# Kernel tuning notes

Measured on AMD Instinct MI355X. Metric: run time of the kernel, lower is better.

The kernel has to match this reference:

```python
import jax, jax.numpy as jnp
import numpy as np

NEG_SLOPE = 0.2  # PyG GATv2Conv default negative_slope


def gatv2_layer(x, Wl, Wr, att, bias, src, dst, N, H, C):
    # x: [N, F_in]; Wl, Wr: [F_in, H*C]; att: [H, C]; bias: [H*C]
    xl = (x @ Wl).reshape(N, H, C)  # source transform (lin_l)
    xr = (x @ Wr).reshape(N, H, C)  # target transform (lin_r)
    # per-edge GATv2 score: a^T LeakyReLU(xl[j] + xr[i])
    e = jax.nn.leaky_relu(xl[src] + xr[dst], NEG_SLOPE)      # [E, H, C]
    logits = jnp.einsum('ehc,hc->eh', e, att)                # [E, H]
    # segment softmax over incoming edges of each destination node
    m = jax.ops.segment_max(logits, dst, num_segments=N)     # [N, H]
    p = jnp.exp(logits - m[dst])                             # [E, H]
    s = jax.ops.segment_sum(p, dst, num_segments=N)          # [N, H]
    alpha = p / s[dst]                                       # [E, H]
    out = jax.ops.segment_sum(xl[src] * alpha[..., None], dst, num_segments=N)  # [N, H, C]
    return out.reshape(N, H * C) + bias


def setup_inputs() -> dict:
    key = jax.random.key(0)
    ks = jax.random.split(key, 12)
    B, N, F_IN = 1, 100000, 128
    E, H, C = 1600000, 4, 16
    D = H * C  # 64
    x = jax.random.normal(ks[0], (B, N, F_IN), dtype=jnp.float32)
    edge_index = jax.random.randint(ks[1], (2, E), 0, N, dtype=jnp.int32)
    def glorot(k, shape):
        fan_in, fan_out = shape[0], shape[1]
        lim = (6.0 / (fan_in + fan_out)) ** 0.5
        return jax.random.uniform(k, shape, jnp.float32, -lim, lim)
    # layer 1: F_IN -> H*C ; layer 2: H*C -> H*C
    W1l = glorot(ks[2], (F_IN, D))
    W1r = glorot(ks[3], (F_IN, D))
    att1 = glorot(ks[4], (H, C))
    b1 = jnp.zeros((D,), jnp.float32)
    W2l = glorot(ks[5], (D, D))
    W2r = glorot(ks[6], (D, D))
    att2 = glorot(ks[7], (H, C))
    b2 = jnp.zeros((D,), jnp.float32)
    return {"x": x, "edge_index": edge_index,
            "W1l": W1l, "W1r": W1r, "att1": att1, "b1": b1,
            "W2l": W2l, "W2r": W2r, "att2": att2, "b2": b2}


def reference(x, edge_index, W1l, W1r, att1, b1, W2l, W2r, att2, b2):
    B, N_per, F = x.shape
    N = B * N_per
    H, C = att1.shape
    h = x.reshape(N, F)
    # PyG GATv2Conv adds self-loops by default
    loops = jnp.arange(N, dtype=edge_index.dtype)
    src = jnp.concatenate([edge_index[0], loops])
    dst = jnp.concatenate([edge_index[1], loops])
    h = jax.nn.relu(gatv2_layer(h, W1l, W1r, att1, b1, src, dst, N, H, C))
    # dropout is identity in eval mode
    h = jax.nn.relu(gatv2_layer(h, W2l, W2r, att2, b2, src, dst, N, H, C))
    return h.reshape(B, N_per, -1)
```

## Files before the change

### kernel.cpp

```cpp
#include <hip/hip_runtime.h>
#include <hip/hip_bf16.h>


typedef unsigned long long u64;

#define NBLK_S 512
#define LOG2E 1.44269504f

template <int CTRL>
__device__ __forceinline__ float add_ror(float v) {
    int r = __builtin_amdgcn_update_dpp(0, __float_as_int(v), CTRL, 0xF, 0xF, true);
    return v + __int_as_float(r);
}
__device__ __forceinline__ float head_sum16(float v) {
    v = add_ror<0x121>(v);
    v = add_ror<0x122>(v);
    v = add_ror<0x124>(v);
    v = add_ror<0x128>(v);
    return v;
}

__global__ void hist_kernel(const int* __restrict__ dst, int* __restrict__ deg, int E) {
    int i = blockIdx.x * blockDim.x + threadIdx.x;
    int stride = gridDim.x * blockDim.x;
    for (; i < E; i += stride) atomicAdd(&deg[dst[i]], 1);
}

__global__ void scan_a(const int* __restrict__ deg, int* __restrict__ incl,
                       int* __restrict__ partials, int n) {
    __shared__ int sm[2][1024];
    int tid = threadIdx.x;
    int i = blockIdx.x * 1024 + tid;
    int v = (i < n) ? deg[i] : 0;
    sm[0][tid] = v;
    __syncthreads();
    int pin = 0;
    #pragma unroll
    for (int ofs = 1; ofs < 1024; ofs <<= 1) {
        int pout = pin ^ 1;
        sm[pout][tid] = sm[pin][tid] + ((tid >= ofs) ? sm[pin][tid - ofs] : 0);
        pin = pout;
        __syncthreads();
    }
    int r = sm[pin][tid];
    if (i < n) incl[i] = r;
    if (tid == 1023) partials[blockIdx.x] = r;
}

__global__ void scan_b(int* partials, int nblk) {
    __shared__ int sm[2][1024];
    int tid = threadIdx.x;
    int v = (tid < nblk) ? partials[tid] : 0;
    sm[0][tid] = v;
    __syncthreads();
    int pin = 0;
    #pragma unroll
    for (int ofs = 1; ofs < 1024; ofs <<= 1) {
        int pout = pin ^ 1;
        sm[pout][tid] = sm[pin][tid] + ((tid >= ofs) ? sm[pin][tid - ofs] : 0);
        pin = pout;
        __syncthreads();
    }
    if (tid < nblk) partials[tid] = sm[pin][tid] - v;
}

__global__ void scan_c(const int* __restrict__ deg, const int* __restrict__ incl,
                       const int* __restrict__ partials, int* __restrict__ offs,
                       int n, int E) {
    int i = blockIdx.x * blockDim.x + threadIdx.x;
    if (i < n) offs[i] = partials[i >> 10] + incl[i] - deg[i];
    if (i == 0) offs[n] = E;
}

__global__ __launch_bounds__(256) void sort_hist(const int* __restrict__ edst,
                                                 int* __restrict__ gh, int E, int nW) {
    __shared__ int h[256];
    for (int i = threadIdx.x; i < nW; i += 256) h[i] = 0;
    __syncthreads();
    const int chunk = (E + NBLK_S - 1) / NBLK_S;
    const int lo = blockIdx.x * chunk;
    const int hi = min(E, lo + chunk);
    for (int i = lo + threadIdx.x; i < hi; i += 256)
        atomicAdd(&h[edst[i] >> 9], 1);
    __syncthreads();
    for (int w = threadIdx.x; w < nW; w += 256)
        gh[w * NBLK_S + blockIdx.x] = h[w];
}

__global__ __launch_bounds__(NBLK_S) void sort_scan(const int* __restrict__ offs,
                                                    int* __restrict__ gh, int N) {
    __shared__ int sm[2][NBLK_S];
    const int w = blockIdx.x;
    const int t = threadIdx.x;
    int v = gh[w * NBLK_S + t];
    sm[0][t] = v;
    __syncthreads();
    int pin = 0;
    #pragma unroll
    for (int ofs = 1; ofs < NBLK_S; ofs <<= 1) {
        int pout = pin ^ 1;
        sm[pout][t] = sm[pin][t] + ((t >= ofs) ? sm[pin][t - ofs] : 0);
        pin = pout;
        __syncthreads();
    }
    gh[w * NBLK_S + t] = offs[w << 9] + sm[pin][t] - v;
}

__global__ __launch_bounds__(256) void sort_place(const int* __restrict__ esrc,
                                                  const int* __restrict__ edst,
                                                  const int* __restrict__ gh,
                                                  u64* __restrict__ pairs, int E, int nW) {
    __shared__ int cur[256];
    for (int i = threadIdx.x; i < nW; i += 256)
        cur[i] = gh[i * NBLK_S + blockIdx.x];
    __syncthreads();
    const int chunk = (E + NBLK_S - 1) / NBLK_S;
    const int lo = blockIdx.x * chunk;
    const int hi = min(E, lo + chunk);
    for (int i = lo + threadIdx.x; i < hi; i += 256) {
        int d = edst[i];
        int s = esrc[i];
        int pos = atomicAdd(&cur[d >> 9], 1);
        pairs[pos] = ((u64)(unsigned)d << 32) | (unsigned)s;
    }
}

__global__ __launch_bounds__(256) void window_scatter(const u64* __restrict__ pairs,
                                                      const int* __restrict__ offs,
                                                      int* __restrict__ srcs, int N) {
    __shared__ int cur[512];
    int w = blockIdx.x;
    int d0 = w << 9;
    int nd = min(512, N - d0);
    for (int i = threadIdx.x; i < nd; i += 256) cur[i] = offs[d0 + i];
    __syncthreads();
    int p0 = offs[d0];
    int p1 = offs[min(d0 + 512, N)];
    for (int idx = p0 + threadIdx.x; idx < p1; idx += 256) {
        u64 pr = pairs[idx];
        int d = (int)(pr >> 32);
        int s = (int)(pr & 0xffffffffu);
        int pos = atomicAdd(&cur[d - d0], 1);
        srcs[pos] = s;
    }
}

#define WIDX(c) ((c) + (((c) >> 5) << 2))
template <int K>
__global__ __launch_bounds__(256) void gemm_lr(const float* __restrict__ X,
                                               const float* __restrict__ Wl,
                                               const float* __restrict__ Wr,
                                               float* __restrict__ xl,
                                               float* __restrict__ xr, int N) {
    constexpr int KT = 64;
    constexpr int LDW = 140;
    constexpr int LDX = KT + 4;
    __shared__ float Ws[KT][LDW];
    __shared__ float Xs[64][LDX];
    const int tid = threadIdx.x;
    const int rbase = blockIdx.x * 64;
    const int tx = tid & 15;
    const int ty = tid >> 4;
    const int c0 = tx * 8;
    const int wc = WIDX(c0);

    float acc[4][8];
    #pragma unroll
    for (int j = 0; j < 4; ++j)
        #pragma unroll
        for (int i = 0; i < 8; ++i) acc[j][i] = 0.f;

    #pragma unroll
    for (int t = 0; t < K / KT; ++t) {
        if (t) __syncthreads();
        for (int f = tid; f < KT * 16; f += 256) {
            int k = f >> 4;
            int c = (f & 15) << 2;
            float4 a = *reinterpret_cast<const float4*>(&Wl[(size_t)(t * KT + k) * 64 + c]);
            float4 b = *reinterpret_cast<const float4*>(&Wr[(size_t)(t * KT + k) * 64 + c]);
            *reinterpret_cast<float4*>(&Ws[k][WIDX(c)]) = a;
            *reinterpret_cast<float4*>(&Ws[k][WIDX(64 + c)]) = b;
        }
        for (int f = tid; f < 64 * (KT / 4); f += 256) {
            int m = f >> 4;
            int k4 = (f & 15) << 2;
            int r = rbase + m;
            float4 v = (r < N) ? *reinterpret_cast<const float4*>(&X[(size_t)r * K + t * KT + k4])
                               : make_float4(0.f, 0.f, 0.f, 0.f);
            *reinterpret_cast<float4*>(&Xs[m][k4]) = v;
        }
        __syncthreads();

        #pragma unroll 2
        for (int k4 = 0; k4 < KT; k4 += 4) {
            float4 xv[4];
            #pragma unroll
            for (int j = 0; j < 4; ++j)
                xv[j] = *reinterpret_cast<const float4*>(&Xs[ty + 16 * j][k4]);
            #pragma unroll
            for (int kk = 0; kk < 4; ++kk) {
                float4 w0 = *reinterpret_cast<const float4*>(&Ws[k4 + kk][wc]);
                float4 w1 = *reinterpret_cast<const float4*>(&Ws[k4 + kk][wc + 4]);
                float w[8] = {w0.x, w0.y, w0.z, w0.w, w1.x, w1.y, w1.z, w1.w};
                #pragma unroll
                for (int j = 0; j < 4; ++j) {
                    float xk = (kk == 0) ? xv[j].x : (kk == 1) ? xv[j].y
                             : (kk == 2) ? xv[j].z : xv[j].w;
                    #pragma unroll
                    for (int i = 0; i < 8; ++i)
                        acc[j][i] = fmaf(xk, w[i], acc[j][i]);
                }
            }
        }
    }

    float* op = (c0 < 64) ? xl : xr;
    const int cc = c0 & 63;
    #pragma unroll
    for (int j = 0; j < 4; ++j) {
        int r = rbase + ty + 16 * j;
        if (r < N) {
            float4 v0 = make_float4(acc[j][0], acc[j][1], acc[j][2], acc[j][3]);
            float4 v1 = make_float4(acc[j][4], acc[j][5], acc[j][6], acc[j][7]);
            *reinterpret_cast<float4*>(&op[(size_t)r * 64 + cc]) = v0;
            *reinterpret_cast<float4*>(&op[(size_t)r * 64 + cc + 4]) = v1;
        }
    }
}

__global__ __launch_bounds__(256) void gat_kernel(const float* __restrict__ xl,
                                                  const float* __restrict__ xr,
                                                  const int* __restrict__ offs,
                                                  const int* __restrict__ srcs,
                                                  const float* __restrict__ att,
                                                  const float* __restrict__ bias,
                                                  float* __restrict__ out, int N) {
    int lane = threadIdx.x & 63;
    int wid = threadIdx.x >> 6;
    int n = blockIdx.x * 4 + wid;
    if (n >= N) return;
    float att_l = att[lane] * LOG2E;
    float b_l = bias[lane];
    float xr_d = xr[(size_t)n * 64 + lane];
    float xls = xl[(size_t)n * 64 + lane];
    float v = xls + xr_d;
    float p = exp2f(head_sum16(att_l * fmaxf(v, 0.2f * v)));
    float s0 = p, s1 = 0.f, s2 = 0.f, s3 = 0.f;
    float o0 = xls * p, o1 = 0.f, o2 = 0.f, o3 = 0.f;
    int e0 = offs[n], e1 = offs[n + 1];
    int j = e0;
    for (; j + 3 < e1; j += 4) {
        int sa = srcs[j], sb = srcs[j + 1], sc = srcs[j + 2], sd = srcs[j + 3];
        float xa = xl[(size_t)sa * 64 + lane];
        float xb = xl[(size_t)sb * 64 + lane];
        float xc = xl[(size_t)sc * 64 + lane];
        float xd = xl[(size_t)sd * 64 + lane];
        float ua = xa + xr_d, ub = xb + xr_d, uc = xc + xr_d, ud = xd + xr_d;
        float pa = exp2f(head_sum16(att_l * fmaxf(ua, 0.2f * ua)));
        float pb = exp2f(head_sum16(att_l * fmaxf(ub, 0.2f * ub)));
        float pc = exp2f(head_sum16(att_l * fmaxf(uc, 0.2f * uc)));
        float pd = exp2f(head_sum16(att_l * fmaxf(ud, 0.2f * ud)));
        s0 += pa; s1 += pb; s2 += pc; s3 += pd;
        o0 = fmaf(xa, pa, o0);
        o1 = fmaf(xb, pb, o1);
        o2 = fmaf(xc, pc, o2);
        o3 = fmaf(xd, pd, o3);
    }
    for (; j < e1; ++j) {
        int sa = srcs[j];
        float xa = xl[(size_t)sa * 64 + lane];
        float ua = xa + xr_d;
        float pa = exp2f(head_sum16(att_l * fmaxf(ua, 0.2f * ua)));
        s1 += pa;
        o1 = fmaf(xa, pa, o1);
    }
    float s = (s0 + s1) + (s2 + s3);
    float o = (o0 + o1) + (o2 + o3);
    out[(size_t)n * 64 + lane] = fmaxf(o / s + b_l, 0.f);
}

extern "C" void kernel_launch(void* const* d_in, const int* in_sizes, int n_in,
                              void* d_out, int out_size, void* d_ws, size_t ws_size,
                              hipStream_t stream) {
    const float* x    = (const float*)d_in[0];
    const int*   edge = (const int*)d_in[1];
    const float* W1l  = (const float*)d_in[2];
    const float* W1r  = (const float*)d_in[3];
    const float* att1 = (const float*)d_in[4];
    const float* b1   = (const float*)d_in[5];
    const float* W2l  = (const float*)d_in[6];
    const float* W2r  = (const float*)d_in[7];
    const float* att2 = (const float*)d_in[8];
    const float* b2   = (const float*)d_in[9];

    const int N = in_sizes[0] / 128;
    const int E = in_sizes[1] / 2;
    const int* esrc = edge;
    const int* edst = edge + E;

    char* ws = (char*)d_ws;
    size_t off = 0;
    auto alloc = [&](size_t bytes) {
        void* p = ws + off;
        off += (bytes + 255) & ~(size_t)255;
        return p;
    };
    float* xl     = (float*)alloc((size_t)N * 64 * 4);
    float* xr     = (float*)alloc((size_t)N * 64 * 4);
    float* h      = (float*)alloc((size_t)N * 64 * 4);
    int* deg      = (int*)alloc((size_t)N * 4);
    int* incl     = (int*)alloc((size_t)N * 4);
    int* offs     = (int*)alloc((size_t)(N + 1) * 4);
    int* partials = (int*)alloc(1024 * 4);
    int* srcs     = (int*)alloc((size_t)E * 4);
    u64* pairs    = (u64*)alloc((size_t)E * 8);
    int* gh       = (int*)alloc((size_t)256 * NBLK_S * 4);
    (void)ws_size;

    hipMemsetAsync(deg, 0, (size_t)N * 4, stream);

    const int nblk = (N + 1023) >> 10;
    const int nW = (N + 511) >> 9;
    hist_kernel<<<1024, 256, 0, stream>>>(edst, deg, E);
    scan_a<<<nblk, 1024, 0, stream>>>(deg, incl, partials, N);
    scan_b<<<1, 1024, 0, stream>>>(partials, nblk);
    scan_c<<<(N + 255) / 256, 256, 0, stream>>>(deg, incl, partials, offs, N, E);
    sort_hist<<<NBLK_S, 256, 0, stream>>>(edst, gh, E, nW);
    sort_scan<<<nW, NBLK_S, 0, stream>>>(offs, gh, N);
    sort_place<<<NBLK_S, 256, 0, stream>>>(esrc, edst, gh, pairs, E, nW);
    window_scatter<<<nW, 256, 0, stream>>>(pairs, offs, srcs, N);

    const int gblk = (N + 63) / 64;
    gemm_lr<128><<<gblk, 256, 0, stream>>>(x, W1l, W1r, xl, xr, N);
    gat_kernel<<<(N + 3) / 4, 256, 0, stream>>>(xl, xr, offs, srcs, att1, b1, h, N);
    gemm_lr<64><<<gblk, 256, 0, stream>>>(h, W2l, W2r, xl, xr, N);
    gat_kernel<<<(N + 3) / 4, 256, 0, stream>>>(xl, xr, offs, srcs, att2, b2, (float*)d_out, N);
}
```

Baseline: 461.5 us.

## Fuse histograms, overlap edge sort with first GEMM, compact pairs, tune GAT gather

```diff
diff --git a/kernel.cpp b/kernel.cpp
--- a/kernel.cpp
+++ b/kernel.cpp
@@ -20,10 +20,23 @@
     return v;
 }
 
-__global__ void hist_kernel(const int* __restrict__ dst, int* __restrict__ deg, int E) {
-    int i = blockIdx.x * blockDim.x + threadIdx.x;
-    int stride = gridDim.x * blockDim.x;
-    for (; i < E; i += stride) atomicAdd(&deg[dst[i]], 1);
+__global__ __launch_bounds__(256) void hist_fused(const int* __restrict__ edst,
+                                                  int* __restrict__ deg,
+                                                  int* __restrict__ gh, int E, int nW) {
+    __shared__ int h[256];
+    for (int i = threadIdx.x; i < 256; i += 256) h[i] = 0;
+    __syncthreads();
+    const int chunk = (E + NBLK_S - 1) / NBLK_S;
+    const int lo = blockIdx.x * chunk;
+    const int hi = min(E, lo + chunk);
+    for (int i = lo + threadIdx.x; i < hi; i += 256) {
+        int d = edst[i];
+        atomicAdd(&deg[d], 1);
+        atomicAdd(&h[d >> 9], 1);
+    }
+    __syncthreads();
+    for (int w = threadIdx.x; w < nW; w += 256)
+        gh[w * NBLK_S + blockIdx.x] = h[w];
 }
 
 __global__ void scan_a(const int* __restrict__ deg, int* __restrict__ incl,
@@ -72,21 +85,6 @@
     if (i == 0) offs[n] = E;
 }
 
-__global__ __launch_bounds__(256) void sort_hist(const int* __restrict__ edst,
-                                                 int* __restrict__ gh, int E, int nW) {
-    __shared__ int h[256];
-    for (int i = threadIdx.x; i < nW; i += 256) h[i] = 0;
-    __syncthreads();
-    const int chunk = (E + NBLK_S - 1) / NBLK_S;
-    const int lo = blockIdx.x * chunk;
-    const int hi = min(E, lo + chunk);
-    for (int i = lo + threadIdx.x; i < hi; i += 256)
-        atomicAdd(&h[edst[i] >> 9], 1);
-    __syncthreads();
-    for (int w = threadIdx.x; w < nW; w += 256)
-        gh[w * NBLK_S + blockIdx.x] = h[w];
-}
-
 __global__ __launch_bounds__(NBLK_S) void sort_scan(const int* __restrict__ offs,
                                                     int* __restrict__ gh, int N) {
     __shared__ int sm[2][NBLK_S];
@@ -106,59 +104,22 @@
     gh[w * NBLK_S + t] = offs[w << 9] + sm[pin][t] - v;
 }
 
-__global__ __launch_bounds__(256) void sort_place(const int* __restrict__ esrc,
-                                                  const int* __restrict__ edst,
-                                                  const int* __restrict__ gh,
-                                                  u64* __restrict__ pairs, int E, int nW) {
-    __shared__ int cur[256];
-    for (int i = threadIdx.x; i < nW; i += 256)
-        cur[i] = gh[i * NBLK_S + blockIdx.x];
-    __syncthreads();
-    const int chunk = (E + NBLK_S - 1) / NBLK_S;
-    const int lo = blockIdx.x * chunk;
-    const int hi = min(E, lo + chunk);
-    for (int i = lo + threadIdx.x; i < hi; i += 256) {
-        int d = edst[i];
-        int s = esrc[i];
-        int pos = atomicAdd(&cur[d >> 9], 1);
-        pairs[pos] = ((u64)(unsigned)d << 32) | (unsigned)s;
-    }
-}
-
-__global__ __launch_bounds__(256) void window_scatter(const u64* __restrict__ pairs,
-                                                      const int* __restrict__ offs,
-                                                      int* __restrict__ srcs, int N) {
-    __shared__ int cur[512];
-    int w = blockIdx.x;
-    int d0 = w << 9;
-    int nd = min(512, N - d0);
-    for (int i = threadIdx.x; i < nd; i += 256) cur[i] = offs[d0 + i];
-    __syncthreads();
-    int p0 = offs[d0];
-    int p1 = offs[min(d0 + 512, N)];
-    for (int idx = p0 + threadIdx.x; idx < p1; idx += 256) {
-        u64 pr = pairs[idx];
-        int d = (int)(pr >> 32);
-        int s = (int)(pr & 0xffffffffu);
-        int pos = atomicAdd(&cur[d - d0], 1);
-        srcs[pos] = s;
-    }
-}
-
 #define WIDX(c) ((c) + (((c) >> 5) << 2))
+#define GEMM_LDS_FLOATS (64 * 140 + 64 * 68)
+
 template <int K>
-__global__ __launch_bounds__(256) void gemm_lr(const float* __restrict__ X,
-                                               const float* __restrict__ Wl,
-                                               const float* __restrict__ Wr,
-                                               float* __restrict__ xl,
-                                               float* __restrict__ xr, int N) {
+__device__ __forceinline__ void gemm_body(int rbase, const float* __restrict__ X,
+                                          const float* __restrict__ Wl,
+                                          const float* __restrict__ Wr,
+                                          float* __restrict__ xl,
+                                          float* __restrict__ xr, int N,
+                                          float* __restrict__ sm) {
     constexpr int KT = 64;
     constexpr int LDW = 140;
     constexpr int LDX = KT + 4;
-    __shared__ float Ws[KT][LDW];
-    __shared__ float Xs[64][LDX];
+    float* Ws = sm;
+    float* Xs = sm + KT * LDW;
     const int tid = threadIdx.x;
-    const int rbase = blockIdx.x * 64;
     const int tx = tid & 15;
     const int ty = tid >> 4;
     const int c0 = tx * 8;
@@ -178,8 +139,8 @@
             int c = (f & 15) << 2;
             float4 a = *reinterpret_cast<const float4*>(&Wl[(size_t)(t * KT + k) * 64 + c]);
             float4 b = *reinterpret_cast<const float4*>(&Wr[(size_t)(t * KT + k) * 64 + c]);
-            *reinterpret_cast<float4*>(&Ws[k][WIDX(c)]) = a;
-            *reinterpret_cast<float4*>(&Ws[k][WIDX(64 + c)]) = b;
+            *reinterpret_cast<float4*>(&Ws[k * LDW + WIDX(c)]) = a;
+            *reinterpret_cast<float4*>(&Ws[k * LDW + WIDX(64 + c)]) = b;
         }
         for (int f = tid; f < 64 * (KT / 4); f += 256) {
             int m = f >> 4;
@@ -187,7 +148,7 @@
             int r = rbase + m;
             float4 v = (r < N) ? *reinterpret_cast<const float4*>(&X[(size_t)r * K + t * KT + k4])
                                : make_float4(0.f, 0.f, 0.f, 0.f);
-            *reinterpret_cast<float4*>(&Xs[m][k4]) = v;
+            *reinterpret_cast<float4*>(&Xs[m * LDX + k4]) = v;
         }
         __syncthreads();
 
@@ -196,11 +157,11 @@
             float4 xv[4];
             #pragma unroll
             for (int j = 0; j < 4; ++j)
-                xv[j] = *reinterpret_cast<const float4*>(&Xs[ty + 16 * j][k4]);
+                xv[j] = *reinterpret_cast<const float4*>(&Xs[(ty + 16 * j) * LDX + k4]);
             #pragma unroll
             for (int kk = 0; kk < 4; ++kk) {
-                float4 w0 = *reinterpret_cast<const float4*>(&Ws[k4 + kk][wc]);
-                float4 w1 = *reinterpret_cast<const float4*>(&Ws[k4 + kk][wc + 4]);
+                float4 w0 = *reinterpret_cast<const float4*>(&Ws[(k4 + kk) * LDW + wc]);
+                float4 w1 = *reinterpret_cast<const float4*>(&Ws[(k4 + kk) * LDW + wc + 4]);
                 float w[8] = {w0.x, w0.y, w0.z, w0.w, w1.x, w1.y, w1.z, w1.w};
                 #pragma unroll
                 for (int j = 0; j < 4; ++j) {
@@ -226,6 +187,77 @@
             *reinterpret_cast<float4*>(&op[(size_t)r * 64 + cc + 4]) = v1;
         }
     }
+}
+
+__global__ __launch_bounds__(256) void place_gemm(const int* __restrict__ esrc,
+                                                  const int* __restrict__ edst,
+                                                  const int* __restrict__ gh,
+                                                  unsigned* __restrict__ pairs,
+                                                  int E, int nW,
+                                                  const float* __restrict__ X,
+                                                  const float* __restrict__ Wl,
+                                                  const float* __restrict__ Wr,
+                                                  float* __restrict__ xl,
+                                                  float* __restrict__ xr, int N) {
+    __shared__ float sm[GEMM_LDS_FLOATS];
+    if (blockIdx.x < NBLK_S) {
+        int* cur = (int*)sm;
+        const int bid = blockIdx.x;
+        for (int i = threadIdx.x; i < nW; i += 256)
+            cur[i] = gh[i * NBLK_S + bid];
+        __syncthreads();
+        const int chunk = (E + NBLK_S - 1) / NBLK_S;
+        const int lo = bid * chunk;
+        const int hi = min(E, lo + chunk);
+        for (int i = lo + threadIdx.x; i < hi; i += 256) {
+            int d = edst[i];
+            int s = esrc[i];
+            int pos = atomicAdd(&cur[d >> 9], 1);
+            pairs[pos] = ((unsigned)(d & 511) << 17) | (unsigned)s;
+        }
+    } else {
+        gemm_body<128>((blockIdx.x - NBLK_S) * 64, X, Wl, Wr, xl, xr, N, sm);
+    }
+}
+
+__global__ __launch_bounds__(256) void scatter_gemm(const unsigned* __restrict__ pairs,
+                                                    const int* __restrict__ offs,
+                                                    int* __restrict__ srcs, int nW, int gemmBase,
+                                                    const float* __restrict__ X,
+                                                    const float* __restrict__ Wl,
+                                                    const float* __restrict__ Wr,
+                                                    float* __restrict__ xl,
+                                                    float* __restrict__ xr, int N) {
+    __shared__ float sm[GEMM_LDS_FLOATS];
+    if ((int)blockIdx.x < nW) {
+        int* cur = (int*)sm;
+        int w = blockIdx.x;
+        int d0 = w << 9;
+        int nd = min(512, N - d0);
+        for (int i = threadIdx.x; i < nd; i += 256) cur[i] = offs[d0 + i];
+        __syncthreads();
+        int p0 = offs[d0];
+        int p1 = offs[min(d0 + 512, N)];
+        for (int idx = p0 + threadIdx.x; idx < p1; idx += 256) {
+            unsigned pr = pairs[idx];
+            int doff = (int)(pr >> 17);
+            int s = (int)(pr & 0x1FFFFu);
+            int pos = atomicAdd(&cur[doff], 1);
+            srcs[pos] = s << 6;
+        }
+    } else {
+        gemm_body<128>((gemmBase + blockIdx.x - nW) * 64, X, Wl, Wr, xl, xr, N, sm);
+    }
+}
+
+template <int K>
+__global__ __launch_bounds__(256) void gemm_lr(const float* __restrict__ X,
+                                               const float* __restrict__ Wl,
+                                               const float* __restrict__ Wr,
+                                               float* __restrict__ xl,
+                                               float* __restrict__ xr, int N) {
+    __shared__ float sm[GEMM_LDS_FLOATS];
+    gemm_body<K>(blockIdx.x * 64, X, Wl, Wr, xl, xr, N, sm);
 }
 
 __global__ __launch_bounds__(256) void gat_kernel(const float* __restrict__ xl,
@@ -239,27 +271,39 @@
     int wid = threadIdx.x >> 6;
     int n = blockIdx.x * 4 + wid;
     if (n >= N) return;
-    float att_l = att[lane] * LOG2E;
+    float a_l = att[lane] * LOG2E;
+    float a1 = 0.6f * a_l;
+    float a2 = 0.4f * a_l;
     float b_l = bias[lane];
-    float xr_d = xr[(size_t)n * 64 + lane];
-    float xls = xl[(size_t)n * 64 + lane];
-    float v = xls + xr_d;
-    float p = exp2f(head_sum16(att_l * fmaxf(v, 0.2f * v)));
+    unsigned bn = (unsigned)n * 64u + (unsigned)lane;
+    float xr_d = xr[bn];
+    float xls = xl[bn];
+    float u = xls + xr_d;
+    float p = exp2f(head_sum16(fmaf(a1, u, a2 * fabsf(u))));
     float s0 = p, s1 = 0.f, s2 = 0.f, s3 = 0.f;
     float o0 = xls * p, o1 = 0.f, o2 = 0.f, o3 = 0.f;
     int e0 = offs[n], e1 = offs[n + 1];
     int j = e0;
+    int ja = min((e0 + 3) & ~3, e1);
+    for (; j < ja; ++j) {
+        unsigned off = (unsigned)srcs[j] + lane;
+        float xa = xl[off];
+        float ua = xa + xr_d;
+        float pa = exp2f(head_sum16(fmaf(a1, ua, a2 * fabsf(ua))));
+        s1 += pa;
+        o1 = fmaf(xa, pa, o1);
+    }
     for (; j + 3 < e1; j += 4) {
-        int sa = srcs[j], sb = srcs[j + 1], sc = srcs[j + 2], sd = srcs[j + 3];
-        float xa = xl[(size_t)sa * 64 + lane];
-        float xb = xl[(size_t)sb * 64 + lane];
-        float xc = xl[(size_t)sc * 64 + lane];
-        float xd = xl[(size_t)sd * 64 + lane];
+        int4 q = *reinterpret_cast<const int4*>(&srcs[j]);
+        float xa = xl[(unsigned)q.x + lane];
+        float xb = xl[(unsigned)q.y + lane];
+        float xc = xl[(unsigned)q.z + lane];
+        float xd = xl[(unsigned)q.w + lane];
         float ua = xa + xr_d, ub = xb + xr_d, uc = xc + xr_d, ud = xd + xr_d;
-        float pa = exp2f(head_sum16(att_l * fmaxf(ua, 0.2f * ua)));
-        float pb = exp2f(head_sum16(att_l * fmaxf(ub, 0.2f * ub)));
-        float pc = exp2f(head_sum16(att_l * fmaxf(uc, 0.2f * uc)));
-        float pd = exp2f(head_sum16(att_l * fmaxf(ud, 0.2f * ud)));
+        float pa = exp2f(head_sum16(fmaf(a1, ua, a2 * fabsf(ua))));
+        float pb = exp2f(head_sum16(fmaf(a1, ub, a2 * fabsf(ub))));
+        float pc = exp2f(head_sum16(fmaf(a1, uc, a2 * fabsf(uc))));
+        float pd = exp2f(head_sum16(fmaf(a1, ud, a2 * fabsf(ud))));
         s0 += pa; s1 += pb; s2 += pc; s3 += pd;
         o0 = fmaf(xa, pa, o0);
         o1 = fmaf(xb, pb, o1);
@@ -267,16 +311,16 @@
         o3 = fmaf(xd, pd, o3);
     }
     for (; j < e1; ++j) {
-        int sa = srcs[j];
-        float xa = xl[(size_t)sa * 64 + lane];
+        unsigned off = (unsigned)srcs[j] + lane;
+        float xa = xl[off];
         float ua = xa + xr_d;
-        float pa = exp2f(head_sum16(att_l * fmaxf(ua, 0.2f * ua)));
+        float pa = exp2f(head_sum16(fmaf(a1, ua, a2 * fabsf(ua))));
         s1 += pa;
         o1 = fmaf(xa, pa, o1);
     }
     float s = (s0 + s1) + (s2 + s3);
     float o = (o0 + o1) + (o2 + o3);
-    out[(size_t)n * 64 + lane] = fmaxf(o / s + b_l, 0.f);
+    out[bn] = fmaxf(o / s + b_l, 0.f);
 }
 
 extern "C" void kernel_launch(void* const* d_in, const int* in_sizes, int n_in,
@@ -313,7 +357,7 @@
     int* offs     = (int*)alloc((size_t)(N + 1) * 4);
     int* partials = (int*)alloc(1024 * 4);
     int* srcs     = (int*)alloc((size_t)E * 4);
-    u64* pairs    = (u64*)alloc((size_t)E * 8);
+    unsigned* pairs = (unsigned*)alloc((size_t)E * 4);
     int* gh       = (int*)alloc((size_t)256 * NBLK_S * 4);
     (void)ws_size;
 
@@ -321,17 +365,19 @@
 
     const int nblk = (N + 1023) >> 10;
     const int nW = (N + 511) >> 9;
-    hist_kernel<<<1024, 256, 0, stream>>>(edst, deg, E);
+    const int gblk = (N + 63) / 64;
+    const int GA = gblk / 2;
+    const int GB = gblk - GA;
+
+    hist_fused<<<NBLK_S, 256, 0, stream>>>(edst, deg, gh, E, nW);
     scan_a<<<nblk, 1024, 0, stream>>>(deg, incl, partials, N);
     scan_b<<<1, 1024, 0, stream>>>(partials, nblk);
     scan_c<<<(N + 255) / 256, 256, 0, stream>>>(deg, incl, partials, offs, N, E);
-    sort_hist<<<NBLK_S, 256, 0, stream>>>(edst, gh, E, nW);
     sort_scan<<<nW, NBLK_S, 0, stream>>>(offs, gh, N);
-    sort_place<<<NBLK_S, 256, 0, stream>>>(esrc, edst, gh, pairs, E, nW);
-    window_scatter<<<nW, 256, 0, stream>>>(pairs, offs, srcs, N);
-
-    const int gblk = (N + 63) / 64;
-    gemm_lr<128><<<gblk, 256, 0, stream>>>(x, W1l, W1r, xl, xr, N);
+    place_gemm<<<NBLK_S + GA, 256, 0, stream>>>(esrc, edst, gh, pairs, E, nW,
+                                                x, W1l, W1r, xl, xr, N);
+    scatter_gemm<<<nW + GB, 256, 0, stream>>>(pairs, offs, srcs, nW, GA,
+                                              x, W1l, W1r, xl, xr, N);
     gat_kernel<<<(N + 3) / 4, 256, 0, stream>>>(xl, xr, offs, srcs, att1, b1, h, N);
     gemm_lr<64><<<gblk, 256, 0, stream>>>(h, W2l, W2r, xl, xr, N);
     gat_kernel<<<(N + 3) / 4, 256, 0, stream>>>(xl, xr, offs, srcs, att2, b2, (float*)d_out, N);
```

New measurement: 460.6 us. No clear change (-0.2%).
